# Kernel tuning notes

Measured on AMD Instinct MI355X. Metric: run time of the kernel, lower is better.

The kernel has to match this reference:

```python
import jax, jax.numpy as jnp
import numpy as np
import math

N, E, C, A, M, B, H = 50000, 600000, 32, 32, 32, 10, 64


def setup_inputs() -> dict:
    key = jax.random.key(0)
    ks = jax.random.split(key, 14)
    f = jnp.float32
    node_input = jax.random.normal(ks[0], (N, C), f)
    node_attr = jax.random.normal(ks[1], (N, A), f)
    node_deg = 1.0 + 31.0 * jax.random.uniform(ks[2], (N, 1), dtype=f)  # degrees >= 1
    edge_src = jax.random.randint(ks[3], (E,), 0, N, jnp.int32)
    edge_dst = jax.random.randint(ks[4], (E,), 0, N, jnp.int32)
    edge_attr = jax.random.normal(ks[5], (E, 9), f)  # SH up to lmax=2: 1+3+5
    edge_length_embedded = jax.random.uniform(ks[6], (E, B), dtype=f)
    w_lin_in = jax.random.normal(ks[7], (C, A, C), f)    # FCTP(Cx0e, Ax0e -> Cx0e)
    w_lin_mask = jax.random.normal(ks[8], (C, A, M), f)  # FCTP scalar block of linear_mask
    w_out0 = jax.random.normal(ks[9], (C, A, M), f)      # linear_output, l=0 block
    w_out1 = jax.random.normal(ks[10], (C, A, M), f)     # l=1 block
    w_out2 = jax.random.normal(ks[11], (C, A, M), f)     # l=2 block
    W0 = jax.random.normal(ks[12], (B, H), f)            # radial net (edge2weight)
    W1 = jax.random.normal(ks[13], (H, 3 * C), f)        # -> tensor_edge.weight_numel = 3C ('uvu', v=1)
    return dict(node_input=node_input, node_attr=node_attr, node_deg=node_deg,
                edge_src=edge_src, edge_dst=edge_dst, edge_attr=edge_attr,
                edge_length_embedded=edge_length_embedded,
                w_lin_in=w_lin_in, w_lin_mask=w_lin_mask,
                w_out0=w_out0, w_out1=w_out1, w_out2=w_out2, W0=W0, W1=W1,
                numb=100, n=8)


def reference(node_input, node_attr, node_deg, edge_src, edge_dst, edge_attr,
              edge_length_embedded, w_lin_in, w_lin_mask, w_out0, w_out1, w_out2,
              W0, W1, numb, n):
    # GraphConvolution.forward with irreps_in=Cx0e, irreps_node_attr=Ax0e,
    # irreps_edge_attr=1x0e+1x1o+1x2e (lmax=2), irreps_out=Mx0e+Mx1o+Mx2e.
    nN = node_input.shape[0]
    inv_ca = 1.0 / math.sqrt(C * A)

    def fctp_scalar(x, z, w):  # FullyConnectedTensorProduct with all-scalar in1/in2
        return jnp.einsum('nu,nv,uvk->nk', x, z, w) * inv_ca

    # linear_input, then node_deg normalization
    h0 = fctp_scalar(node_input, node_attr, w_lin_in)            # [N, C]
    deg_isqrt = 1.0 / jnp.sqrt(node_deg)                          # [N, 1]
    nf = h0 * deg_isqrt
    # linear_mask: only 0e outputs have tp paths (scalars x scalars); 1o/2e are zero
    mask_scalar = fctp_scalar(node_input, node_attr, w_lin_mask)  # [N, M]

    # edge2weight radial MLP (e3nn FullyConnectedNet style: /sqrt(fan_in), silu hidden)
    h = jax.nn.silu(edge_length_embedded @ W0 * (1.0 / math.sqrt(B)))
    ew = h @ W1 * (1.0 / math.sqrt(H))                            # [E, 3C]
    w0e, w1o, w2e = ew[:, :C], ew[:, C:2 * C], ew[:, 2 * C:]

    # tensor_edge: 'uvu' 0e(x)l->l paths: out[u,m] = w[u]*x_src[u]*Y_l[m]
    xs = nf[edge_src]                                             # gather [E, C]
    m0 = (w0e * xs) * edge_attr[:, :1]                            # [E, C]
    m1 = (w1o * xs)[:, :, None] * edge_attr[:, None, 1:4]         # [E, C, 3]
    m2 = (w2e * xs)[:, :, None] * edge_attr[:, None, 4:9]         # [E, C, 5]

    # scatter-reduce to destination nodes, then deg normalization
    a0 = jax.ops.segment_sum(m0, edge_dst, num_segments=nN) * deg_isqrt
    a1 = jax.ops.segment_sum(m1, edge_dst, num_segments=nN) * deg_isqrt[:, :, None]
    a2 = jax.ops.segment_sum(m2, edge_dst, num_segments=nN) * deg_isqrt[:, :, None]

    # linear_output: FCTP(mid, Ax0e -> out); scalar attr mixes multiplicities per l
    out0 = jnp.einsum('nu,nv,uvk->nk', a0, node_attr, w_out0) * inv_ca        # [N, M]
    out1 = jnp.einsum('num,nv,uvk->nkm', a1, node_attr, w_out1) * inv_ca      # [N, M, 3]
    out2 = jnp.einsum('num,nv,uvk->nkm', a2, node_attr, w_out2) * inv_ca      # [N, M, 5]

    # c_s * node_mask + c_x * node_output; output_mask is 1 on 0e, 0 on 1o/2e
    c_s, c_x = math.sin(math.pi / 8), math.cos(math.pi / 8)
    scal = c_s * mask_scalar + c_x * out0
    return jnp.concatenate([scal, out1.reshape(nN, 3 * M), out2.reshape(nN, 5 * M)], axis=1)
```

## Files before the change

kernel.cpp:

```cpp
#include <hip/hip_runtime.h>

#define NC 32
#define NB 10
#define NH 64
#define REC 128

typedef __attribute__((ext_vector_type(8))) short bf16x8;
typedef __attribute__((ext_vector_type(4))) float f32x4;

static __device__ __forceinline__ unsigned short f2bf(float f) {
  union { float f; unsigned u; } v; v.f = f;
  unsigned r = v.u + 0x7fffu + ((v.u >> 16) & 1u);
  return (unsigned short)(r >> 16);
}
static __device__ __forceinline__ float bf2f(unsigned short b) {
  union { unsigned u; float f; } v; v.u = ((unsigned)b) << 16;
  return v.f;
}

__global__ void k_prep(const float* __restrict__ nattr, const float* __restrict__ ndeg,
                       const float* __restrict__ w0, const float* __restrict__ w1,
                       const float* __restrict__ w2, const float* __restrict__ w3,
                       const float* __restrict__ w4, const float* __restrict__ W1g,
                       const int* __restrict__ edst, int* __restrict__ cnt,
                       unsigned short* __restrict__ zb, float* __restrict__ dis,
                       unsigned short* __restrict__ wrp, unsigned short* __restrict__ w1p,
                       int N, int E) {
  int i = blockIdx.x * 256 + threadIdx.x;
  int nz = N * NC;
  if (i < nz) { zb[i] = f2bf(nattr[i]); return; }
  i -= nz;
  if (i < N) { dis[i] = rsqrtf(ndeg[i]); return; }
  i -= N;
  if (i < 5 * 32768) {
    int T = i >> 15, r = i & 32767;
    int t = r >> 9, l = (r >> 3) & 63, b = r & 7;
    int j = t * 16 + (l & 15);
    int u = j >> 5, k = j & 31, v = 8 * (l >> 4) + b;
    const float* w = (T == 0) ? w0 : (T == 1) ? w1 : (T == 2) ? w2 : (T == 3) ? w3 : w4;
    wrp[T * 32768 + (t * 64 + l) * 8 + b] = f2bf(w[u * 1024 + v * 32 + k] * (1.0f / 32.0f));
    return;
  }
  i -= 5 * 32768;
  if (i < 6144) {
    int c = i / 3072, r2 = i % 3072;
    int t = r2 >> 9, l = (r2 >> 3) & 63, b = r2 & 7;
    int k = 32 * c + 8 * (l >> 4) + b, col = 16 * t + (l & 15);
    w1p[i] = f2bf(W1g[k * 96 + col] * 0.125f);
    return;
  }
  i -= 6144;
  if (i < E) atomicAdd(&cnt[edst[i]], 1);
}

__global__ __launch_bounds__(256) void k_nfmask(
    const unsigned short* __restrict__ wrp, const unsigned short* __restrict__ zb,
    const float* __restrict__ x_in, const float* __restrict__ dis,
    float* __restrict__ nf, float* __restrict__ maskb, int N) {
  __shared__ float zw[8 * 1024];
  __shared__ float xl[8][32];
  int tid = threadIdx.x;
  int lane = tid & 63, wv = tid >> 6;
  int nbase = blockIdx.x << 3;

  for (int i = tid; i < 8 * 32; i += 256) xl[i >> 5][i & 31] = x_in[nbase * 32 + i];

  int arow = lane & 15;
  bf16x8 af = {0,0,0,0,0,0,0,0};
  if (arow < 8) af = *(const bf16x8*)(zb + (nbase + arow) * 32 + 8 * (lane >> 4));

  int rb = 4 * (lane >> 4);
  int n = tid >> 5, k = tid & 31;
  for (int T = 0; T < 2; ++T) {
    f32x4 acc[16];
#pragma unroll
    for (int i2 = 0; i2 < 16; ++i2) {
      int t = wv * 16 + i2;
      bf16x8 bfr = *(const bf16x8*)(wrp + ((size_t)T * 32768) + ((size_t)t * 64 + lane) * 8);
      f32x4 z4 = {0.f, 0.f, 0.f, 0.f};
      acc[i2] = __builtin_amdgcn_mfma_f32_16x16x32_bf16(af, bfr, z4, 0, 0, 0);
    }
    __syncthreads();
    if (rb < 8) {
#pragma unroll
      for (int i2 = 0; i2 < 16; ++i2) {
        int col = (wv * 16 + i2) * 16 + (lane & 15);
#pragma unroll
        for (int r = 0; r < 4; ++r) zw[(rb + r) * 1024 + col] = acc[i2][r];
      }
    }
    __syncthreads();
    float s = 0.f;
    const float* zr = &zw[n * 1024];
#pragma unroll
    for (int u = 0; u < 32; ++u) s = fmaf(xl[n][u], zr[u * 32 + k], s);
    int gn = nbase + n;
    if (T == 0) nf[gn * 32 + k] = s * dis[gn];
    else        maskb[gn * 32 + k] = s;
  }
}

__global__ __launch_bounds__(512) void k_scan1(const int* __restrict__ cnt, int* __restrict__ exl,
                                               int* __restrict__ bsum, int n) {
  __shared__ int s[512];
  int t = threadIdx.x;
  int i = blockIdx.x * 512 + t;
  int v = (i < n) ? cnt[i] : 0;
  s[t] = v;
  __syncthreads();
  for (int off = 1; off < 512; off <<= 1) {
    int add = (t >= off) ? s[t - off] : 0;
    __syncthreads();
    s[t] += add;
    __syncthreads();
  }
  if (i < n) exl[i] = s[t] - v;
  if (t == 511) bsum[blockIdx.x] = s[511];
}
__global__ void k_scan2(int* __restrict__ bsum, int nb) {
  __shared__ int s[128];
  int t = threadIdx.x;
  int v = (t < nb) ? bsum[t] : 0;
  s[t] = v;
  __syncthreads();
  for (int off = 1; off < 128; off <<= 1) {
    int add = (t >= off) ? s[t - off] : 0;
    __syncthreads();
    s[t] += add;
    __syncthreads();
  }
  if (t < nb) bsum[t] = s[t] - v;
}
__global__ void k_scan3(int* __restrict__ off, const int* __restrict__ bbase,
                        int* __restrict__ cur, int N, int E) {
  int i = blockIdx.x * 256 + threadIdx.x;
  if (i < N) {
    int o = off[i] + bbase[i >> 9];
    off[i] = o;
    cur[i] = o;
  } else if (i == N) {
    off[N] = E;
  }
}
__global__ void k_fill(const int* __restrict__ dst, int* __restrict__ cur,
                       int* __restrict__ pos, int E) {
  int i = blockIdx.x * 256 + threadIdx.x;
  if (i < E) pos[i] = atomicAdd(&cur[dst[i]], 1);
}

#define TS 136
__global__ __launch_bounds__(256) void k_mlp(const float* __restrict__ el,
                                             const float* __restrict__ W0g,
                                             const unsigned short* __restrict__ w1p,
                                             const int* __restrict__ pos,
                                             const int* __restrict__ esrc,
                                             const float* __restrict__ eattr,
                                             unsigned short* __restrict__ recs, int E) {
  __shared__ float w0s[NB * NH];
  __shared__ __align__(16) unsigned short tile[64 * TS];
  __shared__ int posl[64];
  int tid = threadIdx.x;
  int ebase = blockIdx.x * 64;
  for (int i = tid; i < NB * NH; i += 256) w0s[i] = W0g[i] * 0.31622776601683794f;
  if (tid < 64) posl[tid] = pos[ebase + tid];

  for (int i = tid; i < 64 * 10; i += 256) {
    int le = i / 10, c = i - le * 10;
    int e = ebase + le;
    if (c < 9) tile[le * TS + 96 + c] = f2bf(eattr[(size_t)e * 9 + c]);
    else       tile[le * TS + 105] = (unsigned short)esrc[e];
  }
  __syncthreads();

  int lane = tid & 63, wv = tid >> 6;
  int eloc0 = wv * 16;
  int erow = ebase + eloc0 + (lane & 15);
  float elr[NB];
#pragma unroll
  for (int b = 0; b < NB; ++b) elr[b] = el[erow * NB + b];
  int g8 = 8 * (lane >> 4);
  bf16x8 afr[2];
#pragma unroll
  for (int c = 0; c < 2; ++c) {
#pragma unroll
    for (int b = 0; b < 8; ++b) {
      int j = 32 * c + g8 + b;
      float p = 0.f;
#pragma unroll
      for (int q = 0; q < NB; ++q) p = fmaf(elr[q], w0s[q * NH + j], p);
      float h = p / (1.f + __expf(-p));
      afr[c][b] = (short)f2bf(h);
    }
  }
  f32x4 acc[6];
#pragma unroll
  for (int t = 0; t < 6; ++t) { f32x4 z4 = {0.f, 0.f, 0.f, 0.f}; acc[t] = z4; }
#pragma unroll
  for (int c = 0; c < 2; ++c) {
#pragma unroll
    for (int t = 0; t < 6; ++t) {
      bf16x8 bfr = *(const bf16x8*)(w1p + ((c * 6 + t) * 64 + lane) * 8);
      acc[t] = __builtin_amdgcn_mfma_f32_16x16x32_bf16(afr[c], bfr, acc[t], 0, 0, 0);
    }
  }
  int rb = 4 * (lane >> 4);
#pragma unroll
  for (int t = 0; t < 6; ++t) {
    int col = 16 * t + (lane & 15);
#pragma unroll
    for (int r = 0; r < 4; ++r) tile[(eloc0 + rb + r) * TS + col] = f2bf(acc[t][r]);
  }
  __syncthreads();
  for (int ch = tid; ch < 64 * 16; ch += 256) {
    int le = ch >> 4, seg = ch & 15;
    size_t p = (size_t)posl[le];
    *(uint4*)(recs + p * REC + seg * 8) = *(const uint4*)(&tile[le * TS + seg * 8]);
  }
}

__global__ __launch_bounds__(256) void k_gather(
    const int* __restrict__ off, const unsigned short* __restrict__ recs,
    const float* __restrict__ nf, const float* __restrict__ dis,
    float* __restrict__ a_all, int N) {
  int hw = blockIdx.x * 4 + (threadIdx.x >> 6);
  int lane = threadIdx.x & 63;
  int u = lane & 31, half = lane >> 5;
  if (hw >= N) return;
  int beg = off[hw], end = off[hw + 1];
  float a0 = 0, a1x = 0, a1y = 0, a1z = 0, b0 = 0, b1 = 0, b2 = 0, b3 = 0, b4 = 0;
  float xs_next = 0.f;
  int p0 = beg + half;
  if (p0 < end) {
    int s0 = recs[(size_t)p0 * REC + 105];
    xs_next = nf[(size_t)s0 * 32 + u];
  }
  for (int p = p0; p < end; p += 2) {
    float xs = xs_next;
    int p2 = p + 2;
    if (p2 < end) {
      int s2 = recs[(size_t)p2 * REC + 105];
      xs_next = nf[(size_t)s2 * 32 + u];
    }
    const unsigned short* r = recs + (size_t)p * REC;
    float w0 = bf2f(r[u]), w1 = bf2f(r[32 + u]), w2 = bf2f(r[64 + u]);
    float t0 = w0 * xs, t1 = w1 * xs, t2 = w2 * xs;
    a0  = fmaf(t0, bf2f(r[96]), a0);
    a1x = fmaf(t1, bf2f(r[97]), a1x);
    a1y = fmaf(t1, bf2f(r[98]), a1y);
    a1z = fmaf(t1, bf2f(r[99]), a1z);
    b0  = fmaf(t2, bf2f(r[100]), b0);
    b1  = fmaf(t2, bf2f(r[101]), b1);
    b2  = fmaf(t2, bf2f(r[102]), b2);
    b3  = fmaf(t2, bf2f(r[103]), b3);
    b4  = fmaf(t2, bf2f(r[104]), b4);
  }
  a0 += __shfl_xor(a0, 32, 64);  a1x += __shfl_xor(a1x, 32, 64);
  a1y += __shfl_xor(a1y, 32, 64); a1z += __shfl_xor(a1z, 32, 64);
  b0 += __shfl_xor(b0, 32, 64);  b1 += __shfl_xor(b1, 32, 64);
  b2 += __shfl_xor(b2, 32, 64);  b3 += __shfl_xor(b3, 32, 64);
  b4 += __shfl_xor(b4, 32, 64);
  if (half == 0) {
    float d = dis[hw];
    float* ar = a_all + (size_t)hw * 288;
    ar[0 * 32 + u] = a0 * d;
    ar[1 * 32 + u] = a1x * d;
    ar[2 * 32 + u] = a1y * d;
    ar[3 * 32 + u] = a1z * d;
    ar[4 * 32 + u] = b0 * d;
    ar[5 * 32 + u] = b1 * d;
    ar[6 * 32 + u] = b2 * d;
    ar[7 * 32 + u] = b3 * d;
    ar[8 * 32 + u] = b4 * d;
  }
}

__global__ __launch_bounds__(256) void k_out(
    const unsigned short* __restrict__ wrp, const unsigned short* __restrict__ zb,
    const float* __restrict__ a_all, const float* __restrict__ maskb,
    float* __restrict__ out, int N) {
  __shared__ float zw[8 * 1024];
  __shared__ float xl[8][9][32];
  int tid = threadIdx.x;
  int lane = tid & 63, wv = tid >> 6;
  int nbase = blockIdx.x << 3;

  for (int i = tid; i < 8 * 288; i += 256) {
    int n2 = i / 288, rem = i - n2 * 288;
    xl[n2][rem >> 5][rem & 31] = a_all[(size_t)(nbase + n2) * 288 + rem];
  }

  int arow = lane & 15;
  bf16x8 af = {0,0,0,0,0,0,0,0};
  if (arow < 8) af = *(const bf16x8*)(zb + (nbase + arow) * 32 + 8 * (lane >> 4));

  const float c_s = 0.3826834323650898f;
  const float c_x = 0.9238795325112867f;
  int rb = 4 * (lane >> 4);
  int n = tid >> 5, k = tid & 31;
  const int nmT[3] = {1, 3, 5};
  const int moff[3] = {0, 1, 4};
  const int ooff[3] = {0, 32, 128};

  for (int T = 0; T < 3; ++T) {
    f32x4 acc[16];
#pragma unroll
    for (int i2 = 0; i2 < 16; ++i2) {
      int t = wv * 16 + i2;
      bf16x8 bfr = *(const bf16x8*)(wrp + ((size_t)(2 + T) * 32768) + ((size_t)t * 64 + lane) * 8);
      f32x4 z4 = {0.f, 0.f, 0.f, 0.f};
      acc[i2] = __builtin_amdgcn_mfma_f32_16x16x32_bf16(af, bfr, z4, 0, 0, 0);
    }
    __syncthreads();
    if (rb < 8) {
#pragma unroll
      for (int i2 = 0; i2 < 16; ++i2) {
        int col = (wv * 16 + i2) * 16 + (lane & 15);
#pragma unroll
        for (int r = 0; r < 4; ++r) zw[(rb + r) * 1024 + col] = acc[i2][r];
      }
    }
    __syncthreads();
    const float* zr = &zw[n * 1024];
    int gn = nbase + n;
    int nm = nmT[T];
    for (int m = 0; m < nm; ++m) {
      float s = 0.f;
      const float* xr = xl[n][moff[T] + m];
#pragma unroll
      for (int u = 0; u < 32; ++u) s = fmaf(xr[u], zr[u * 32 + k], s);
      if (T == 0) s = c_x * s + c_s * maskb[(size_t)gn * 32 + k];
      out[(size_t)gn * 288 + ooff[T] + k * nm + m] = s;
    }
  }
}

extern "C" void kernel_launch(void* const* d_in, const int* in_sizes, int n_in,
                              void* d_out, int out_size, void* d_ws, size_t ws_size,
                              hipStream_t stream) {
  const float* node_input = (const float*)d_in[0];
  const float* node_attr  = (const float*)d_in[1];
  const float* node_deg   = (const float*)d_in[2];
  const int*   edge_src   = (const int*)d_in[3];
  const int*   edge_dst   = (const int*)d_in[4];
  const float* edge_attr  = (const float*)d_in[5];
  const float* el_emb     = (const float*)d_in[6];
  const float* w_lin_in   = (const float*)d_in[7];
  const float* w_lin_mask = (const float*)d_in[8];
  const float* w_out0     = (const float*)d_in[9];
  const float* w_out1     = (const float*)d_in[10];
  const float* w_out2     = (const float*)d_in[11];
  const float* W0         = (const float*)d_in[12];
  const float* W1         = (const float*)d_in[13];
  int N = in_sizes[0] / 32;
  int E = in_sizes[3];
  float* out = (float*)d_out;

  char* p = (char*)d_ws;
  auto carve = [&](size_t bytes) { char* r = p; p += (bytes + 255) & ~(size_t)255; return r; };
  unsigned short* recs = (unsigned short*)carve((size_t)E * REC * 2);
  float* a_all        = (float*)carve((size_t)N * 288 * 4);
  float* nf           = (float*)carve((size_t)N * 32 * 4);
  float* maskb        = (float*)carve((size_t)N * 32 * 4);
  unsigned short* zb  = (unsigned short*)carve((size_t)N * 32 * 2);
  float* dis          = (float*)carve((size_t)N * 4);
  unsigned short* wrp = (unsigned short*)carve(5 * 32768 * 2);
  unsigned short* w1p = (unsigned short*)carve(6144 * 2);
  int* cnt            = (int*)carve((size_t)N * 4);
  int* off            = (int*)carve((size_t)(N + 1) * 4);
  int* cur            = (int*)carve((size_t)N * 4);
  int* pos            = (int*)carve((size_t)E * 4);
  int* bsum           = (int*)carve(1024);

  hipMemsetAsync(cnt, 0, (size_t)N * 4, stream);

  int tot = N * 32 + N + 5 * 32768 + 6144 + E;
  k_prep<<<(tot + 255) / 256, 256, 0, stream>>>(node_attr, node_deg, w_lin_in, w_lin_mask,
                                                w_out0, w_out1, w_out2, W1, edge_dst, cnt,
                                                zb, dis, wrp, w1p, N, E);

  k_nfmask<<<N / 8, 256, 0, stream>>>(wrp, zb, node_input, dis, nf, maskb, N);

  int nb1 = (N + 511) / 512;
  k_scan1<<<nb1, 512, 0, stream>>>(cnt, off, bsum, N);
  k_scan2<<<1, 128, 0, stream>>>(bsum, nb1);
  k_scan3<<<(N + 1 + 255) / 256, 256, 0, stream>>>(off, bsum, cur, N, E);
  k_fill<<<(E + 255) / 256, 256, 0, stream>>>(edge_dst, cur, pos, E);

  k_mlp<<<E / 64, 256, 0, stream>>>(el_emb, W0, w1p, pos, edge_src, edge_attr, recs, E);
  k_gather<<<(N + 3) / 4, 256, 0, stream>>>(off, recs, nf, dis, a_all, N);

  k_out<<<N / 8, 256, 0, stream>>>(wrp, zb, a_all, maskb, out, N);
}
```

Measured before the change: 502.1 us.

## Fold the bilinear node tensor products into single fp16 MFMA contractions

Result: faster. 428.3 us (-14.7%).

```diff
diff --git a/kernel.cpp b/kernel.cpp
--- a/kernel.cpp
+++ b/kernel.cpp
@@ -7,6 +7,7 @@
 
 typedef __attribute__((ext_vector_type(8))) short bf16x8;
 typedef __attribute__((ext_vector_type(4))) float f32x4;
+typedef _Float16 f16x8 __attribute__((ext_vector_type(8)));
 
 static __device__ __forceinline__ unsigned short f2bf(float f) {
   union { float f; unsigned u; } v; v.f = f;
@@ -23,22 +24,22 @@
                        const float* __restrict__ w2, const float* __restrict__ w3,
                        const float* __restrict__ w4, const float* __restrict__ W1g,
                        const int* __restrict__ edst, int* __restrict__ cnt,
-                       unsigned short* __restrict__ zb, float* __restrict__ dis,
-                       unsigned short* __restrict__ wrp, unsigned short* __restrict__ w1p,
+                       _Float16* __restrict__ zh, float* __restrict__ dis,
+                       _Float16* __restrict__ wrp, unsigned short* __restrict__ w1p,
                        int N, int E) {
   int i = blockIdx.x * 256 + threadIdx.x;
   int nz = N * NC;
-  if (i < nz) { zb[i] = f2bf(nattr[i]); return; }
+  if (i < nz) { zh[i] = (_Float16)nattr[i]; return; }
   i -= nz;
   if (i < N) { dis[i] = rsqrtf(ndeg[i]); return; }
   i -= N;
   if (i < 5 * 32768) {
     int T = i >> 15, r = i & 32767;
-    int t = r >> 9, l = (r >> 3) & 63, b = r & 7;
-    int j = t * 16 + (l & 15);
-    int u = j >> 5, k = j & 31, v = 8 * (l >> 4) + b;
+    int tile = r >> 9, l = (r >> 3) & 63, b = r & 7;
+    int kk = tile >> 1, t = tile & 1;
+    int v = 8 * (l >> 4) + b, k = t * 16 + (l & 15);
     const float* w = (T == 0) ? w0 : (T == 1) ? w1 : (T == 2) ? w2 : (T == 3) ? w3 : w4;
-    wrp[T * 32768 + (t * 64 + l) * 8 + b] = f2bf(w[u * 1024 + v * 32 + k] * (1.0f / 32.0f));
+    wrp[T * 32768 + (tile * 64 + l) * 8 + b] = (_Float16)(w[kk * 1024 + v * 32 + k] * (1.0f / 32.0f));
     return;
   }
   i -= 5 * 32768;
@@ -53,51 +54,51 @@
   if (i < E) atomicAdd(&cnt[edst[i]], 1);
 }
 
-__global__ __launch_bounds__(256) void k_nfmask(
-    const unsigned short* __restrict__ wrp, const unsigned short* __restrict__ zb,
+__global__ __launch_bounds__(64) void k_nfmask(
+    const _Float16* __restrict__ wrp, const _Float16* __restrict__ zh,
     const float* __restrict__ x_in, const float* __restrict__ dis,
     float* __restrict__ nf, float* __restrict__ maskb, int N) {
-  __shared__ float zw[8 * 1024];
-  __shared__ float xl[8][32];
-  int tid = threadIdx.x;
-  int lane = tid & 63, wv = tid >> 6;
-  int nbase = blockIdx.x << 3;
-
-  for (int i = tid; i < 8 * 32; i += 256) xl[i >> 5][i & 31] = x_in[nbase * 32 + i];
-
-  int arow = lane & 15;
-  bf16x8 af = {0,0,0,0,0,0,0,0};
-  if (arow < 8) af = *(const bf16x8*)(zb + (nbase + arow) * 32 + 8 * (lane >> 4));
-
-  int rb = 4 * (lane >> 4);
-  int n = tid >> 5, k = tid & 31;
-  for (int T = 0; T < 2; ++T) {
-    f32x4 acc[16];
-#pragma unroll
-    for (int i2 = 0; i2 < 16; ++i2) {
-      int t = wv * 16 + i2;
-      bf16x8 bfr = *(const bf16x8*)(wrp + ((size_t)T * 32768) + ((size_t)t * 64 + lane) * 8);
-      f32x4 z4 = {0.f, 0.f, 0.f, 0.f};
-      acc[i2] = __builtin_amdgcn_mfma_f32_16x16x32_bf16(af, bfr, z4, 0, 0, 0);
-    }
-    __syncthreads();
-    if (rb < 8) {
-#pragma unroll
-      for (int i2 = 0; i2 < 16; ++i2) {
-        int col = (wv * 16 + i2) * 16 + (lane & 15);
-#pragma unroll
-        for (int r = 0; r < 4; ++r) zw[(rb + r) * 1024 + col] = acc[i2][r];
+  __shared__ float xs[32 * 17];
+  int lane = threadIdx.x;
+  int nbase = blockIdx.x * 16;
+  for (int i = lane; i < 512; i += 64) {
+    int row = i >> 5, kk = i & 31;
+    xs[kk * 17 + row] = x_in[(nbase + row) * 32 + kk];
+  }
+  f16x8 zf = *(const f16x8*)(zh + (nbase + (lane & 15)) * 32 + 8 * (lane >> 4));
+  __syncthreads();
+
+  f32x4 acc[2][2];
+#pragma unroll
+  for (int T = 0; T < 2; ++T)
+#pragma unroll
+    for (int t = 0; t < 2; ++t) { f32x4 z4 = {0.f,0.f,0.f,0.f}; acc[T][t] = z4; }
+
+  int row16 = lane & 15;
+#pragma unroll
+  for (int kk = 0; kk < 32; ++kk) {
+    _Float16 xh = (_Float16)xs[kk * 17 + row16];
+    f16x8 af;
+#pragma unroll
+    for (int b = 0; b < 8; ++b) af[b] = zf[b] * xh;
+#pragma unroll
+    for (int T = 0; T < 2; ++T)
+#pragma unroll
+      for (int t = 0; t < 2; ++t) {
+        f16x8 bf = *(const f16x8*)(wrp + (size_t)T * 32768 + ((kk * 2 + t) * 64 + lane) * 8);
+        acc[T][t] = __builtin_amdgcn_mfma_f32_16x16x32_f16(af, bf, acc[T][t], 0, 0, 0);
       }
-    }
-    __syncthreads();
-    float s = 0.f;
-    const float* zr = &zw[n * 1024];
-#pragma unroll
-    for (int u = 0; u < 32; ++u) s = fmaf(xl[n][u], zr[u * 32 + k], s);
-    int gn = nbase + n;
-    if (T == 0) nf[gn * 32 + k] = s * dis[gn];
-    else        maskb[gn * 32 + k] = s;
-  }
+  }
+  int rg = lane >> 4, c0 = lane & 15;
+#pragma unroll
+  for (int t = 0; t < 2; ++t)
+#pragma unroll
+    for (int r = 0; r < 4; ++r) {
+      int gn = nbase + 4 * rg + r;
+      int k = t * 16 + c0;
+      nf[gn * 32 + k] = acc[0][t][r] * dis[gn];
+      maskb[gn * 32 + k] = acc[1][t][r];
+    }
 }
 
 __global__ __launch_bounds__(512) void k_scan1(const int* __restrict__ cnt, int* __restrict__ exl,
@@ -274,64 +275,62 @@
   }
 }
 
-__global__ __launch_bounds__(256) void k_out(
-    const unsigned short* __restrict__ wrp, const unsigned short* __restrict__ zb,
+__global__ __launch_bounds__(64) void k_out(
+    const _Float16* __restrict__ wrp, const _Float16* __restrict__ zh,
     const float* __restrict__ a_all, const float* __restrict__ maskb,
     float* __restrict__ out, int N) {
-  __shared__ float zw[8 * 1024];
-  __shared__ float xl[8][9][32];
-  int tid = threadIdx.x;
-  int lane = tid & 63, wv = tid >> 6;
-  int nbase = blockIdx.x << 3;
-
-  for (int i = tid; i < 8 * 288; i += 256) {
-    int n2 = i / 288, rem = i - n2 * 288;
-    xl[n2][rem >> 5][rem & 31] = a_all[(size_t)(nbase + n2) * 288 + rem];
-  }
-
-  int arow = lane & 15;
-  bf16x8 af = {0,0,0,0,0,0,0,0};
-  if (arow < 8) af = *(const bf16x8*)(zb + (nbase + arow) * 32 + 8 * (lane >> 4));
+  __shared__ float xs[288 * 17];
+  int lane = threadIdx.x;
+  int nbase = blockIdx.x * 16;
+  for (int i = lane; i < 16 * 288; i += 64) {
+    int row = i / 288, c = i - row * 288;
+    xs[c * 17 + row] = a_all[(size_t)(nbase + row) * 288 + c];
+  }
+  f16x8 zf = *(const f16x8*)(zh + (nbase + (lane & 15)) * 32 + 8 * (lane >> 4));
+  __syncthreads();
+
+  f32x4 acc[9][2];
+#pragma unroll
+  for (int m = 0; m < 9; ++m)
+#pragma unroll
+    for (int t = 0; t < 2; ++t) { f32x4 z4 = {0.f,0.f,0.f,0.f}; acc[m][t] = z4; }
+
+  int row16 = lane & 15;
+  for (int kk = 0; kk < 32; ++kk) {
+    f16x8 bfr[3][2];
+#pragma unroll
+    for (int T = 0; T < 3; ++T)
+#pragma unroll
+      for (int t = 0; t < 2; ++t)
+        bfr[T][t] = *(const f16x8*)(wrp + (size_t)(2 + T) * 32768 + ((kk * 2 + t) * 64 + lane) * 8);
+#pragma unroll
+    for (int m = 0; m < 9; ++m) {
+      _Float16 xh = (_Float16)xs[(m * 32 + kk) * 17 + row16];
+      f16x8 af;
+#pragma unroll
+      for (int b = 0; b < 8; ++b) af[b] = zf[b] * xh;
+      int T = (m == 0) ? 0 : (m < 4) ? 1 : 2;
+      acc[m][0] = __builtin_amdgcn_mfma_f32_16x16x32_f16(af, bfr[T][0], acc[m][0], 0, 0, 0);
+      acc[m][1] = __builtin_amdgcn_mfma_f32_16x16x32_f16(af, bfr[T][1], acc[m][1], 0, 0, 0);
+    }
+  }
 
   const float c_s = 0.3826834323650898f;
   const float c_x = 0.9238795325112867f;
-  int rb = 4 * (lane >> 4);
-  int n = tid >> 5, k = tid & 31;
-  const int nmT[3] = {1, 3, 5};
-  const int moff[3] = {0, 1, 4};
-  const int ooff[3] = {0, 32, 128};
-
-  for (int T = 0; T < 3; ++T) {
-    f32x4 acc[16];
-#pragma unroll
-    for (int i2 = 0; i2 < 16; ++i2) {
-      int t = wv * 16 + i2;
-      bf16x8 bfr = *(const bf16x8*)(wrp + ((size_t)(2 + T) * 32768) + ((size_t)t * 64 + lane) * 8);
-      f32x4 z4 = {0.f, 0.f, 0.f, 0.f};
-      acc[i2] = __builtin_amdgcn_mfma_f32_16x16x32_bf16(af, bfr, z4, 0, 0, 0);
-    }
-    __syncthreads();
-    if (rb < 8) {
-#pragma unroll
-      for (int i2 = 0; i2 < 16; ++i2) {
-        int col = (wv * 16 + i2) * 16 + (lane & 15);
-#pragma unroll
-        for (int r = 0; r < 4; ++r) zw[(rb + r) * 1024 + col] = acc[i2][r];
-      }
-    }
-    __syncthreads();
-    const float* zr = &zw[n * 1024];
-    int gn = nbase + n;
-    int nm = nmT[T];
-    for (int m = 0; m < nm; ++m) {
-      float s = 0.f;
-      const float* xr = xl[n][moff[T] + m];
-#pragma unroll
-      for (int u = 0; u < 32; ++u) s = fmaf(xr[u], zr[u * 32 + k], s);
-      if (T == 0) s = c_x * s + c_s * maskb[(size_t)gn * 32 + k];
-      out[(size_t)gn * 288 + ooff[T] + k * nm + m] = s;
-    }
-  }
+  int rg = lane >> 4, c0 = lane & 15;
+#pragma unroll
+  for (int t = 0; t < 2; ++t)
+#pragma unroll
+    for (int r = 0; r < 4; ++r) {
+      int gn = nbase + 4 * rg + r;
+      int k = t * 16 + c0;
+      float* orow = out + (size_t)gn * 288;
+      orow[k] = c_x * acc[0][t][r] + c_s * maskb[(size_t)gn * 32 + k];
+#pragma unroll
+      for (int m = 0; m < 3; ++m) orow[32 + k * 3 + m] = acc[1 + m][t][r];
+#pragma unroll
+      for (int m = 0; m < 5; ++m) orow[128 + k * 5 + m] = acc[4 + m][t][r];
+    }
 }
 
 extern "C" void kernel_launch(void* const* d_in, const int* in_sizes, int n_in,
@@ -361,9 +360,9 @@
   float* a_all        = (float*)carve((size_t)N * 288 * 4);
   float* nf           = (float*)carve((size_t)N * 32 * 4);
   float* maskb        = (float*)carve((size_t)N * 32 * 4);
-  unsigned short* zb  = (unsigned short*)carve((size_t)N * 32 * 2);
+  _Float16* zh        = (_Float16*)carve((size_t)N * 32 * 2);
   float* dis          = (float*)carve((size_t)N * 4);
-  unsigned short* wrp = (unsigned short*)carve(5 * 32768 * 2);
+  _Float16* wrp       = (_Float16*)carve(5 * 32768 * 2);
   unsigned short* w1p = (unsigned short*)carve(6144 * 2);
   int* cnt            = (int*)carve((size_t)N * 4);
   int* off            = (int*)carve((size_t)(N + 1) * 4);
@@ -376,9 +375,9 @@
   int tot = N * 32 + N + 5 * 32768 + 6144 + E;
   k_prep<<<(tot + 255) / 256, 256, 0, stream>>>(node_attr, node_deg, w_lin_in, w_lin_mask,
                                                 w_out0, w_out1, w_out2, W1, edge_dst, cnt,
-                                                zb, dis, wrp, w1p, N, E);
-
-  k_nfmask<<<N / 8, 256, 0, stream>>>(wrp, zb, node_input, dis, nf, maskb, N);
+                                                zh, dis, wrp, w1p, N, E);
+
+  k_nfmask<<<N / 16, 64, 0, stream>>>(wrp, zh, node_input, dis, nf, maskb, N);
 
   int nb1 = (N + 511) / 512;
   k_scan1<<<nb1, 512, 0, stream>>>(cnt, off, bsum, N);
@@ -389,5 +388,5 @@
   k_mlp<<<E / 64, 256, 0, stream>>>(el_emb, W0, w1p, pos, edge_src, edge_attr, recs, E);
   k_gather<<<(N + 3) / 4, 256, 0, stream>>>(off, recs, nf, dis, a_all, N);
 
-  k_out<<<N / 8, 256, 0, stream>>>(wrp, zb, a_all, maskb, out, N);
-}
+  k_out<<<N / 16, 64, 0, stream>>>(wrp, zh, a_all, maskb, out, N);
+}
```
